# Kernel tuning notes

Measured on AMD Instinct MI355X. Metric: run time of the kernel, lower is better.

The kernel has to match this reference:

```python
import jax, jax.numpy as jnp
import numpy as np

NEG_SLOPE = 0.2
NUM_GRAPHS = 1000


def gatv2_layer(x, src, dst, Wl, bl, Wr, br, att, bias, heads, outc, concat):
    # PyG GATv2Conv (eval mode, dropout inactive, self-loops already appended)
    N = x.shape[0]
    xl = (x @ Wl + bl).reshape(N, heads, outc)   # source transform
    xr = (x @ Wr + br).reshape(N, heads, outc)   # target transform
    e = jax.nn.leaky_relu(xl[src] + xr[dst], NEG_SLOPE)      # [E,H,C]
    logit = jnp.einsum('ehc,hc->eh', e, att)                  # [E,H]
    m = jax.ops.segment_max(logit, dst, num_segments=N)      # segment softmax over dst
    ex = jnp.exp(logit - m[dst])
    denom = jax.ops.segment_sum(ex, dst, num_segments=N)
    alpha = ex / denom[dst]                                   # [E,H]
    out = jax.ops.segment_sum(xl[src] * alpha[:, :, None], dst, num_segments=N)  # [N,H,C]
    out = out.reshape(N, heads * outc) if concat else out.mean(axis=1)
    return out + bias


def _glorot(key, shape, scale=0.05):
    return jax.random.normal(key, shape, dtype=jnp.float32) * scale


def setup_inputs() -> dict:
    key = jax.random.key(0)
    ks = jax.random.split(key, 24)
    N, E = 50000, 800000
    Din, Hc, H, Dout = 64, 64, 4, 128
    inp = {
        'x': jax.random.normal(ks[0], (N, Din), dtype=jnp.float32),
        'edge_index': jax.random.randint(ks[1], (2, E), 0, N, dtype=jnp.int32),
        'batch': jnp.sort(jax.random.randint(ks[2], (N,), 0, NUM_GRAPHS, dtype=jnp.int32)),
        # layer 1: Din -> H*Hc (concat)
        'Wl1': _glorot(ks[3], (Din, H * Hc)), 'bl1': jnp.zeros((H * Hc,), jnp.float32),
        'Wr1': _glorot(ks[4], (Din, H * Hc)), 'br1': jnp.zeros((H * Hc,), jnp.float32),
        'att1': _glorot(ks[5], (H, Hc)), 'b1': jnp.zeros((H * Hc,), jnp.float32),
        # layer 2: H*Hc -> H*Hc (concat)
        'Wl2': _glorot(ks[6], (H * Hc, H * Hc)), 'bl2': jnp.zeros((H * Hc,), jnp.float32),
        'Wr2': _glorot(ks[7], (H * Hc, H * Hc)), 'br2': jnp.zeros((H * Hc,), jnp.float32),
        'att2': _glorot(ks[8], (H, Hc)), 'b2': jnp.zeros((H * Hc,), jnp.float32),
        # layer 3: H*Hc -> Dout, 1 head, concat=False
        'Wl3': _glorot(ks[9], (H * Hc, Dout)), 'bl3': jnp.zeros((Dout,), jnp.float32),
        'Wr3': _glorot(ks[10], (H * Hc, Dout)), 'br3': jnp.zeros((Dout,), jnp.float32),
        'att3': _glorot(ks[11], (1, Dout)), 'b3': jnp.zeros((Dout,), jnp.float32),
    }
    return inp


def reference(x, edge_index, batch, Wl1, bl1, Wr1, br1, att1, b1,
              Wl2, bl2, Wr2, br2, att2, b2, Wl3, bl3, Wr3, br3, att3, b3):
    N = x.shape[0]
    loops = jnp.arange(N, dtype=edge_index.dtype)
    src = jnp.concatenate([edge_index[0], loops])  # add_self_loops=True
    dst = jnp.concatenate([edge_index[1], loops])
    h = gatv2_layer(x, src, dst, Wl1, bl1, Wr1, br1, att1, b1, 4, 64, True)
    h = jax.nn.elu(h)
    h = gatv2_layer(h, src, dst, Wl2, bl2, Wr2, br2, att2, b2, 4, 64, True)
    h = jax.nn.elu(h)
    h = gatv2_layer(h, src, dst, Wl3, bl3, Wr3, br3, att3, b3, 1, 128, False)
    # global mean pool over graphs
    sums = jax.ops.segment_sum(h, batch, num_segments=NUM_GRAPHS)
    cnt = jax.ops.segment_sum(jnp.ones((N,), h.dtype), batch, num_segments=NUM_GRAPHS)
    return sums / jnp.clip(cnt, 1.0)[:, None]
```

## Files before the change

kernel.cpp:

```cpp
#include <hip/hip_runtime.h>
#include <math.h>

#define NEG_SLOPE 0.2f

typedef _Float16 half8 __attribute__((ext_vector_type(8)));
typedef _Float16 half4 __attribute__((ext_vector_type(4)));
typedef _Float16 half2v __attribute__((ext_vector_type(2)));
typedef float    f32x4 __attribute__((ext_vector_type(4)));
typedef float    fvec4 __attribute__((ext_vector_type(4)));
typedef float    fvec2 __attribute__((ext_vector_type(2)));

__global__ void k_count(const int* __restrict__ dst, int E, int N, int* __restrict__ cnt){
  int i = blockIdx.x*blockDim.x + threadIdx.x;
  if (i < E) atomicAdd(&cnt[dst[i]], 1);
  else if (i < E + N) atomicAdd(&cnt[i - E], 1);
}

__global__ void k_scan_block(const int* __restrict__ cnt, int* __restrict__ ex,
                             int* __restrict__ bsum, int N){
  __shared__ int tmp[256];
  int t = threadIdx.x;
  int i = blockIdx.x*256 + t;
  int v = (i < N) ? cnt[i] : 0;
  tmp[t] = v; __syncthreads();
  for (int off = 1; off < 256; off <<= 1){
    int u = (t >= off) ? tmp[t-off] : 0;
    __syncthreads();
    tmp[t] += u;
    __syncthreads();
  }
  if (i < N) ex[i] = tmp[t] - v;
  if (t == 255) bsum[blockIdx.x] = tmp[255];
}

__global__ void k_scan_tops(int* __restrict__ bsum, int nb){
  __shared__ int tmp[256];
  int t = threadIdx.x;
  int v = (t < nb) ? bsum[t] : 0;
  tmp[t] = v; __syncthreads();
  for (int off = 1; off < 256; off <<= 1){
    int u = (t >= off) ? tmp[t-off] : 0;
    __syncthreads();
    tmp[t] += u;
    __syncthreads();
  }
  if (t < nb) bsum[t] = tmp[t] - v;
}

__global__ void k_scan_add(int* __restrict__ row_start, const int* __restrict__ bsum,
                           int N, int total){
  int i = blockIdx.x*256 + threadIdx.x;
  if (i < N) row_start[i] += bsum[blockIdx.x];
  if (i == 0) row_start[N] = total;
}

__global__ void k_scatter(const int* __restrict__ src, const int* __restrict__ dst,
                          int E, int N, const int* __restrict__ row_start,
                          int* __restrict__ cursor, int* __restrict__ edge_src){
  int i = blockIdx.x*blockDim.x + threadIdx.x;
  if (i < E){
    int d = dst[i];
    int p = atomicAdd(&cursor[d], 1);
    edge_src[row_start[d] + p] = src[i];
  } else if (i < E + N){
    int n = i - E;
    int p = atomicAdd(&cursor[n], 1);
    edge_src[row_start[n] + p] = n;
  }
}

__global__ void k_splitW(const float* __restrict__ W, _Float16* __restrict__ WT,
                         int K, int Nw){
  int id = blockIdx.x*blockDim.x + threadIdx.x;
  if (id >= K*Nw) return;
  int n = id / K, k = id % K;
  float w = W[(size_t)k*Nw + n];
  _Float16 h = (_Float16)w;
  _Float16 l = (_Float16)(w - (float)h);
  size_t base = (size_t)n*2*K;
  WT[base + k]     = h;
  WT[base + K + k] = l;
}

__global__ void k_split_x(const float* __restrict__ x, _Float16* __restrict__ X16,
                          int N, int K){
  int id = blockIdx.x*blockDim.x + threadIdx.x;
  int per = K/8;
  if (id >= N*per) return;
  int rr = id / per, c = (id % per)*8;
  fvec4 f0 = *(const fvec4*)&x[(size_t)rr*K + c];
  fvec4 f1 = *(const fvec4*)&x[(size_t)rr*K + c + 4];
  half8 hh, hl;
  #pragma unroll
  for (int q = 0; q < 4; ++q){
    _Float16 h0 = (_Float16)f0[q];
    hh[q] = h0; hl[q] = (_Float16)(f0[q] - (float)h0);
    _Float16 h1 = (_Float16)f1[q];
    hh[4+q] = h1; hl[4+q] = (_Float16)(f1[q] - (float)h1);
  }
  *(half8*)&X16[(size_t)rr*2*K + c]     = hh;
  *(half8*)&X16[(size_t)rr*2*K + K + c] = hl;
}

__global__ __launch_bounds__(256, 2)
void k_gemm_split(const _Float16* __restrict__ A16, const _Float16* __restrict__ WT,
                  const float* __restrict__ biasL, const float* __restrict__ biasR,
                  _Float16* __restrict__ XL, _Float16* __restrict__ XR,
                  int M, int K, int NwHalf, int gy, int qq, int rr){
  __shared__ _Float16 sAh[128*72];
  __shared__ _Float16 sAl[128*72];
  __shared__ _Float16 sWh[128*72];
  __shared__ _Float16 sWl[128*72];
  const int tid  = threadIdx.x;
  const int lane = tid & 63;
  const int wid  = tid >> 6;
  const int wm   = wid >> 1, wn = wid & 1;

  const int h   = blockIdx.x;
  const int xcd = h & 7, idx = h >> 3;
  const int l   = xcd*qq + (xcd < rr ? xcd : rr) + idx;
  const int bx  = l / gy, by = l - bx*gy;
  const int m0  = bx * 128;
  const int n0  = by * 128;
  const int lda = 2*K;

  f32x4 acc[4][4];
  #pragma unroll
  for (int i = 0; i < 4; ++i)
    #pragma unroll
    for (int j = 0; j < 4; ++j)
      acc[i][j] = (f32x4){0.f,0.f,0.f,0.f};

  const int l15 = lane & 15;
  const int lhi = lane >> 4;

  const int nc = K/64;
  for (int c = 0; c < nc; ++c){
    const int kA = c*64;
    #pragma unroll
    for (int it = 0; it < 4; ++it){
      int idx2 = it*256 + tid;
      int r = idx2 >> 3, c8 = idx2 & 7;
      int gr = m0 + r;
      half8 vh = (half8)(_Float16)0.f, vl = (half8)(_Float16)0.f;
      if (gr < M){
        vh = *(const half8*)&A16[(size_t)gr*lda + kA + c8*8];
        vl = *(const half8*)&A16[(size_t)gr*lda + K + kA + c8*8];
      }
      *(half8*)&sAh[r*72 + c8*8] = vh;
      *(half8*)&sAl[r*72 + c8*8] = vl;
      int wr = n0 + r;
      *(half8*)&sWh[r*72 + c8*8] = *(const half8*)&WT[(size_t)wr*lda + kA + c8*8];
      *(half8*)&sWl[r*72 + c8*8] = *(const half8*)&WT[(size_t)wr*lda + K + kA + c8*8];
    }
    __syncthreads();
    #pragma unroll
    for (int ks = 0; ks < 64; ks += 32){
      half8 ah[4], al[4], bh[4], bl[4];
      #pragma unroll
      for (int fm = 0; fm < 4; ++fm){
        ah[fm] = *(const half8*)&sAh[(wm*64 + fm*16 + l15)*72 + ks + 8*lhi];
        al[fm] = *(const half8*)&sAl[(wm*64 + fm*16 + l15)*72 + ks + 8*lhi];
      }
      #pragma unroll
      for (int fn = 0; fn < 4; ++fn){
        bh[fn] = *(const half8*)&sWh[(wn*64 + fn*16 + l15)*72 + ks + 8*lhi];
        bl[fn] = *(const half8*)&sWl[(wn*64 + fn*16 + l15)*72 + ks + 8*lhi];
      }
      #pragma unroll
      for (int fm = 0; fm < 4; ++fm)
        #pragma unroll
        for (int fn = 0; fn < 4; ++fn)
          acc[fm][fn] = __builtin_amdgcn_mfma_f32_16x16x32_f16(ah[fm], bh[fn], acc[fm][fn], 0, 0, 0);
      #pragma unroll
      for (int fm = 0; fm < 4; ++fm)
        #pragma unroll
        for (int fn = 0; fn < 4; ++fn)
          acc[fm][fn] = __builtin_amdgcn_mfma_f32_16x16x32_f16(al[fm], bh[fn], acc[fm][fn], 0, 0, 0);
      #pragma unroll
      for (int fm = 0; fm < 4; ++fm)
        #pragma unroll
        for (int fn = 0; fn < 4; ++fn)
          acc[fm][fn] = __builtin_amdgcn_mfma_f32_16x16x32_f16(ah[fm], bl[fn], acc[fm][fn], 0, 0, 0);
    }
    __syncthreads();
  }
  const bool isR = (n0 >= NwHalf);
  const float* bias = isR ? biasR : biasL;
  _Float16* Xo = isR ? XR : XL;
  const int nbase = isR ? (n0 - NwHalf) : n0;
  #pragma unroll
  for (int fm = 0; fm < 4; ++fm){
    #pragma unroll
    for (int fn = 0; fn < 4; ++fn){
      int cc = nbase + wn*64 + fn*16 + l15;
      float bv = bias[cc];
      #pragma unroll
      for (int q = 0; q < 4; ++q){
        int row = m0 + wm*64 + fm*16 + lhi*4 + q;
        if (row < M) Xo[(size_t)row*NwHalf + cc] = (_Float16)(acc[fm][fn][q] + bv);
      }
    }
  }
}

template<int HC, int C, int SPLIT>
__global__ __launch_bounds__(256) void k_gat_agg(const _Float16* __restrict__ xl,
                                                 const _Float16* __restrict__ xr,
                                                 const float* __restrict__ att,
                                                 const float* __restrict__ bias,
                                                 const int* __restrict__ row_start,
                                                 const int* __restrict__ edge_src,
                                                 void* __restrict__ outp,
                                                 int N, int apply_elu){
  constexpr int VEC   = 8;
  constexpr int LPE   = HC/VEC;
  constexpr int EPW   = 64/LPE;
  constexpr int GROUP = C/VEC;
  const float M_INIT = -1.0e30f, T_INACT = -2.0e30f, THR = 11.54f;

  int wid = (int)(((size_t)blockIdx.x * blockDim.x + threadIdx.x) >> 6);
  int lane = threadIdx.x & 63;
  if (wid >= N) return;
  const int h  = lane / LPE;
  const int li = lane % LPE;
  const int ch = (li/GROUP)*C + (li%GROUP)*VEC;

  const _Float16 s16 = (_Float16)NEG_SLOPE;
  const half2v slope2 = {s16, s16};

  half2v attv2[4], xrr2[4];
  {
    fvec4 a0 = *(const fvec4*)&att[ch];
    fvec4 a1 = *(const fvec4*)&att[ch+4];
    const float L2E = 1.4426950408889634f;
    attv2[0][0]=(_Float16)(a0[0]*L2E); attv2[0][1]=(_Float16)(a0[1]*L2E);
    attv2[1][0]=(_Float16)(a0[2]*L2E); attv2[1][1]=(_Float16)(a0[3]*L2E);
    attv2[2][0]=(_Float16)(a1[0]*L2E); attv2[2][1]=(_Float16)(a1[1]*L2E);
    attv2[3][0]=(_Float16)(a1[2]*L2E); attv2[3][1]=(_Float16)(a1[3]*L2E);
    half8 hv = *(const half8*)&xr[(unsigned)(wid*HC) + ch];
    #pragma unroll
    for (int p = 0; p < 4; ++p){ xrr2[p][0] = hv[2*p]; xrr2[p][1] = hv[2*p+1]; }
  }

  float acc[VEC];
  #pragma unroll
  for (int q = 0; q < VEC; ++q) acc[q] = 0.f;
  float m = M_INIT, s = 0.f;

  const int e0   = row_start[wid];
  const int ecnt = row_start[wid+1] - e0;
  const _Float16* xlb = xl + ch;

  auto rowload = [&](int sn)->half8 {
    return *(const half8*)(xlb + (unsigned)(sn*HC));
  };
  auto logit1 = [&](half8 x8)->float{
    float t = 0.f;
    #pragma unroll
    for (int p = 0; p < 4; ++p){
      half2v xp; xp[0] = x8[2*p]; xp[1] = x8[2*p+1];
      half2v v  = xp + xrr2[p];
      half2v lv = __builtin_elementwise_max(v, v*slope2);
      t = __builtin_amdgcn_fdot2(lv, attv2[p], t, false);
    }
    #pragma unroll
    for (int off = GROUP/2; off > 0; off >>= 1)
      t += __shfl_xor(t, off, 64);
    return t;
  };
  auto update2 = [&](float ta, float tb, half8 xa, half8 xb){
    float pm = fmaxf(ta, tb);
    if (__all(pm <= m + THR)){
      float pa = __builtin_amdgcn_exp2f(ta - m);
      float pb = __builtin_amdgcn_exp2f(tb - m);
      s += pa + pb;
      #pragma unroll
      for (int q = 0; q < VEC; ++q)
        acc[q] = fmaf(pa, (float)xa[q], fmaf(pb, (float)xb[q], acc[q]));
    } else {
      float nm = fmaxf(pm, m);
      float wo = __builtin_amdgcn_exp2f(m - nm);
      float pa = __builtin_amdgcn_exp2f(ta - nm);
      float pb = __builtin_amdgcn_exp2f(tb - nm);
      s = fmaf(s, wo, pa + pb);
      m = nm;
      #pragma unroll
      for (int q = 0; q < VEC; ++q)
        acc[q] = fmaf(pa, (float)xa[q], fmaf(pb, (float)xb[q], acc[q]*wo));
    }
  };

  int base = e0 + h;
  const int R = ecnt / (2*EPW);
  for (int r = 0; r < R; ++r, base += 2*EPW){
    int sa = edge_src[base];
    int sb = edge_src[base + EPW];
    half8 xa = rowload(sa);
    half8 xb = rowload(sb);
    float ta = logit1(xa);
    float tb = logit1(xb);
    update2(ta, tb, xa, xb);
  }
  if (2*EPW*R < ecnt){
    const int last = e0 + ecnt;
    bool a1 = base < last, a2 = base + EPW < last;
    int sa = a1 ? edge_src[base] : 0;
    int sb = a2 ? edge_src[base + EPW] : 0;
    half8 xa = rowload(sa);
    half8 xb = rowload(sb);
    float ta = logit1(xa); ta = a1 ? ta : T_INACT;
    float tb = logit1(xb); tb = a2 ? tb : T_INACT;
    update2(ta, tb, xa, xb);
  }

  #pragma unroll
  for (int off = LPE; off < 64; off <<= 1){
    float mo = __shfl_xor(m, off, 64);
    float so = __shfl_xor(s, off, 64);
    float M  = fmaxf(m, mo);
    float w  = __builtin_amdgcn_exp2f(m  - M);
    float wo = __builtin_amdgcn_exp2f(mo - M);
    s = s*w + so*wo;
    #pragma unroll
    for (int q = 0; q < VEC; ++q)
      acc[q] = acc[q]*w + __shfl_xor(acc[q], off, 64)*wo;
    m = M;
  }

  if (h == 0){
    float inv = 1.f / s;
    fvec4 b0 = *(const fvec4*)&bias[ch];
    fvec4 b1 = *(const fvec4*)&bias[ch+4];
    float ov[VEC];
    #pragma unroll
    for (int q = 0; q < VEC; ++q){
      float o = acc[q]*inv + (q < 4 ? b0[q] : b1[q-4]);
      if (apply_elu) o = (o > 0.f) ? o : (__expf(o) - 1.f);
      ov[q] = o;
    }
    if constexpr (SPLIT){
      _Float16* o16 = (_Float16*)outp;
      half8 hh, hl;
      #pragma unroll
      for (int q = 0; q < VEC; ++q){
        _Float16 hv = (_Float16)ov[q];
        hh[q] = hv; hl[q] = (_Float16)(ov[q] - (float)hv);
      }
      *(half8*)&o16[(unsigned)(wid*2*HC) + ch]      = hh;
      *(half8*)&o16[(unsigned)(wid*2*HC) + HC + ch] = hl;
    } else {
      float* o32 = (float*)outp;
      *(fvec4*)&o32[(unsigned)(wid*HC) + ch]     = (fvec4){ov[0],ov[1],ov[2],ov[3]};
      *(fvec4*)&o32[(unsigned)(wid*HC) + ch + 4] = (fvec4){ov[4],ov[5],ov[6],ov[7]};
    }
  }
}

__global__ void k_pool(const float* __restrict__ h, const int* __restrict__ batch,
                       float* __restrict__ pool, int* __restrict__ gcnt, int N){
  int wid = (int)(((size_t)blockIdx.x * blockDim.x + threadIdx.x) >> 6);
  int lane = threadIdx.x & 63;
  if (wid >= N) return;
  int g = batch[wid];
  #pragma unroll
  for (int j = 0; j < 2; ++j)
    atomicAdd(&pool[(size_t)g*128 + j*64 + lane], h[(size_t)wid*128 + j*64 + lane]);
  if (lane == 0) atomicAdd(&gcnt[g], 1);
}

__global__ void k_pool_div(const float* __restrict__ pool, const int* __restrict__ gcnt,
                           float* __restrict__ out, int total){
  int i = blockIdx.x*blockDim.x + threadIdx.x;
  if (i < total) out[i] = pool[i] / fmaxf((float)gcnt[i >> 7], 1.f);
}

extern "C" void kernel_launch(void* const* d_in, const int* in_sizes, int n_in,
                              void* d_out, int out_size, void* d_ws, size_t ws_size,
                              hipStream_t stream){
  const float* x    = (const float*)d_in[0];
  const int*   ei   = (const int*)  d_in[1];
  const int*   batch= (const int*)  d_in[2];
  const float* Wl1  = (const float*)d_in[3];
  const float* bl1  = (const float*)d_in[4];
  const float* Wr1  = (const float*)d_in[5];
  const float* br1  = (const float*)d_in[6];
  const float* att1 = (const float*)d_in[7];
  const float* b1   = (const float*)d_in[8];
  const float* Wl2  = (const float*)d_in[9];
  const float* bl2  = (const float*)d_in[10];
  const float* Wr2  = (const float*)d_in[11];
  const float* br2  = (const float*)d_in[12];
  const float* att2 = (const float*)d_in[13];
  const float* b2   = (const float*)d_in[14];
  const float* Wl3  = (const float*)d_in[15];
  const float* bl3  = (const float*)d_in[16];
  const float* Wr3  = (const float*)d_in[17];
  const float* br3  = (const float*)d_in[18];
  const float* att3 = (const float*)d_in[19];
  const float* b3   = (const float*)d_in[20];

  int N  = in_sizes[2];
  int E  = in_sizes[1] / 2;
  int NG = out_size / 128;
  const int* esrc = ei;
  const int* edst = ei + E;
  int Mpad = ((N + 127)/128)*128;

  size_t off = 0;
  char* base = (char*)d_ws;
  auto alloc = [&](size_t bytes)->void*{
    void* p = base + off;
    off += (bytes + 255) & ~(size_t)255;
    return p;
  };
  _Float16* XL  = (_Float16*)alloc((size_t)Mpad*256*sizeof(_Float16));
  _Float16* XR  = (_Float16*)alloc((size_t)Mpad*256*sizeof(_Float16));
  _Float16* Hsp = (_Float16*)alloc((size_t)Mpad*512*sizeof(_Float16));
  _Float16* X16 = (_Float16*)alloc((size_t)Mpad*128*sizeof(_Float16));
  float*    Hb32= (float*)   alloc((size_t)Mpad*128*sizeof(float));
  _Float16* WT  = (_Float16*)alloc((size_t)512*512*sizeof(_Float16));
  int* row_start = (int*)alloc(((size_t)N+1)*sizeof(int));
  int* edge_src  = (int*)alloc((size_t)(E+N)*sizeof(int));
  int* cnt       = (int*)alloc((size_t)N*sizeof(int));
  int* bsum      = (int*)alloc(256*sizeof(int));
  float* pool    = (float*)alloc((size_t)NG*128*sizeof(float));
  int* gcnt      = (int*)alloc((size_t)NG*sizeof(int));
  (void)ws_size; (void)n_in;

  int EN = E + N;
  int nb = (N + 255) / 256;

  hipMemsetAsync(cnt, 0, (size_t)N*sizeof(int), stream);
  k_count<<<(EN+255)/256, 256, 0, stream>>>(edst, E, N, cnt);
  k_scan_block<<<nb, 256, 0, stream>>>(cnt, row_start, bsum, N);
  k_scan_tops<<<1, 256, 0, stream>>>(bsum, nb);
  k_scan_add<<<nb, 256, 0, stream>>>(row_start, bsum, N, EN);
  hipMemsetAsync(cnt, 0, (size_t)N*sizeof(int), stream);
  k_scatter<<<(EN+255)/256, 256, 0, stream>>>(esrc, edst, E, N, row_start, cnt, edge_src);

  dim3 blk(256);
  int agg_blocks = (N + 3) / 4;
  int gx = Mpad/128;
  int G1 = gx*4;
  int G3 = gx*2;

  k_splitW<<<(64*256+255)/256, blk, 0, stream>>>(Wl1, WT,           64, 256);
  k_splitW<<<(64*256+255)/256, blk, 0, stream>>>(Wr1, WT + 256*128, 64, 256);
  k_split_x<<<((N*8)+255)/256, blk, 0, stream>>>(x, X16, N, 64);
  k_gemm_split<<<G1, blk, 0, stream>>>(X16, WT, bl1, br1, XL, XR, N, 64, 256, 4, G1/8, G1%8);
  k_gat_agg<256,64,1><<<agg_blocks, blk, 0, stream>>>(XL, XR, att1, b1, row_start, edge_src, Hsp, N, 1);

  k_splitW<<<(256*256+255)/256, blk, 0, stream>>>(Wl2, WT,           256, 256);
  k_splitW<<<(256*256+255)/256, blk, 0, stream>>>(Wr2, WT + 256*512, 256, 256);
  k_gemm_split<<<G1, blk, 0, stream>>>(Hsp, WT, bl2, br2, XL, XR, N, 256, 256, 4, G1/8, G1%8);
  k_gat_agg<256,64,1><<<agg_blocks, blk, 0, stream>>>(XL, XR, att2, b2, row_start, edge_src, Hsp, N, 1);

  k_splitW<<<(256*128+255)/256, blk, 0, stream>>>(Wl3, WT,           256, 128);
  k_splitW<<<(256*128+255)/256, blk, 0, stream>>>(Wr3, WT + 128*512, 256, 128);
  k_gemm_split<<<G3, blk, 0, stream>>>(Hsp, WT, bl3, br3, XL, XR, N, 256, 128, 2, G3/8, G3%8);
  k_gat_agg<128,128,0><<<agg_blocks, blk, 0, stream>>>(XL, XR, att3, b3, row_start, edge_src, Hb32, N, 0);

  hipMemsetAsync(pool, 0, (size_t)NG*128*sizeof(float), stream);
  hipMemsetAsync(gcnt, 0, (size_t)NG*sizeof(int), stream);
  k_pool<<<agg_blocks, blk, 0, stream>>>(Hb32, batch, pool, gcnt, N);
  k_pool_div<<<(NG*128+255)/256, 256, 0, stream>>>(pool, gcnt, (float*)d_out, NG*128);
}
```

Baseline: 500.9 us.

## Drop activation split-precision, fuse pooling into last aggregation, merge weight-split launches

Activations are now stored as a single fp16 copy instead of an fp16 hi/lo pair, so the GEMM runs two MFMA passes instead of three and reads half the A data. Weights keep their hi/lo split. The final GAT aggregation atomically accumulates straight into the pooled buffer, with the bias added in the divide step, which removes the fp32 intermediate and the separate pool kernel. The two weight-split launches per layer are merged into one. The cost is lower accuracy on activations and more atomic contention on the pool buffer.

```diff
diff --git a/kernel.cpp b/kernel.cpp
--- a/kernel.cpp
+++ b/kernel.cpp
@@ -69,37 +69,37 @@
   }
 }
 
-__global__ void k_splitW(const float* __restrict__ W, _Float16* __restrict__ WT,
-                         int K, int Nw){
+__global__ void k_splitW2(const float* __restrict__ WL, const float* __restrict__ WR,
+                          _Float16* __restrict__ WT, int K, int Nw){
   int id = blockIdx.x*blockDim.x + threadIdx.x;
-  if (id >= K*Nw) return;
-  int n = id / K, k = id % K;
+  if (id >= 2*K*Nw) return;
+  int half = id / (K*Nw);
+  int rem  = id - half*K*Nw;
+  int n = rem / K, k = rem % K;
+  const float* W = half ? WR : WL;
   float w = W[(size_t)k*Nw + n];
   _Float16 h = (_Float16)w;
   _Float16 l = (_Float16)(w - (float)h);
-  size_t base = (size_t)n*2*K;
+  size_t base = (size_t)(half*Nw + n)*2*K;
   WT[base + k]     = h;
   WT[base + K + k] = l;
 }
 
-__global__ void k_split_x(const float* __restrict__ x, _Float16* __restrict__ X16,
-                          int N, int K){
+__global__ void k_cvt_x(const float* __restrict__ x, _Float16* __restrict__ X16,
+                        int N, int K){
   int id = blockIdx.x*blockDim.x + threadIdx.x;
   int per = K/8;
   if (id >= N*per) return;
   int rr = id / per, c = (id % per)*8;
   fvec4 f0 = *(const fvec4*)&x[(size_t)rr*K + c];
   fvec4 f1 = *(const fvec4*)&x[(size_t)rr*K + c + 4];
-  half8 hh, hl;
+  half8 hh;
   #pragma unroll
   for (int q = 0; q < 4; ++q){
-    _Float16 h0 = (_Float16)f0[q];
-    hh[q] = h0; hl[q] = (_Float16)(f0[q] - (float)h0);
-    _Float16 h1 = (_Float16)f1[q];
-    hh[4+q] = h1; hl[4+q] = (_Float16)(f1[q] - (float)h1);
-  }
-  *(half8*)&X16[(size_t)rr*2*K + c]     = hh;
-  *(half8*)&X16[(size_t)rr*2*K + K + c] = hl;
+    hh[q]   = (_Float16)f0[q];
+    hh[4+q] = (_Float16)f1[q];
+  }
+  *(half8*)&X16[(size_t)rr*K + c] = hh;
 }
 
 __global__ __launch_bounds__(256, 2)
@@ -107,8 +107,7 @@
                   const float* __restrict__ biasL, const float* __restrict__ biasR,
                   _Float16* __restrict__ XL, _Float16* __restrict__ XR,
                   int M, int K, int NwHalf, int gy, int qq, int rr){
-  __shared__ _Float16 sAh[128*72];
-  __shared__ _Float16 sAl[128*72];
+  __shared__ _Float16 sA [128*72];
   __shared__ _Float16 sWh[128*72];
   __shared__ _Float16 sWl[128*72];
   const int tid  = threadIdx.x;
@@ -122,7 +121,7 @@
   const int bx  = l / gy, by = l - bx*gy;
   const int m0  = bx * 128;
   const int n0  = by * 128;
-  const int lda = 2*K;
+  const int ldw = 2*K;
 
   f32x4 acc[4][4];
   #pragma unroll
@@ -142,26 +141,20 @@
       int idx2 = it*256 + tid;
       int r = idx2 >> 3, c8 = idx2 & 7;
       int gr = m0 + r;
-      half8 vh = (half8)(_Float16)0.f, vl = (half8)(_Float16)0.f;
-      if (gr < M){
-        vh = *(const half8*)&A16[(size_t)gr*lda + kA + c8*8];
-        vl = *(const half8*)&A16[(size_t)gr*lda + K + kA + c8*8];
-      }
-      *(half8*)&sAh[r*72 + c8*8] = vh;
-      *(half8*)&sAl[r*72 + c8*8] = vl;
+      half8 va = (half8)(_Float16)0.f;
+      if (gr < M) va = *(const half8*)&A16[(size_t)gr*K + kA + c8*8];
+      *(half8*)&sA[r*72 + c8*8] = va;
       int wr = n0 + r;
-      *(half8*)&sWh[r*72 + c8*8] = *(const half8*)&WT[(size_t)wr*lda + kA + c8*8];
-      *(half8*)&sWl[r*72 + c8*8] = *(const half8*)&WT[(size_t)wr*lda + K + kA + c8*8];
+      *(half8*)&sWh[r*72 + c8*8] = *(const half8*)&WT[(size_t)wr*ldw + kA + c8*8];
+      *(half8*)&sWl[r*72 + c8*8] = *(const half8*)&WT[(size_t)wr*ldw + K + kA + c8*8];
     }
     __syncthreads();
     #pragma unroll
     for (int ks = 0; ks < 64; ks += 32){
-      half8 ah[4], al[4], bh[4], bl[4];
-      #pragma unroll
-      for (int fm = 0; fm < 4; ++fm){
-        ah[fm] = *(const half8*)&sAh[(wm*64 + fm*16 + l15)*72 + ks + 8*lhi];
-        al[fm] = *(const half8*)&sAl[(wm*64 + fm*16 + l15)*72 + ks + 8*lhi];
-      }
+      half8 a[4], bh[4], bl[4];
+      #pragma unroll
+      for (int fm = 0; fm < 4; ++fm)
+        a[fm] = *(const half8*)&sA[(wm*64 + fm*16 + l15)*72 + ks + 8*lhi];
       #pragma unroll
       for (int fn = 0; fn < 4; ++fn){
         bh[fn] = *(const half8*)&sWh[(wn*64 + fn*16 + l15)*72 + ks + 8*lhi];
@@ -171,17 +164,12 @@
       for (int fm = 0; fm < 4; ++fm)
         #pragma unroll
         for (int fn = 0; fn < 4; ++fn)
-          acc[fm][fn] = __builtin_amdgcn_mfma_f32_16x16x32_f16(ah[fm], bh[fn], acc[fm][fn], 0, 0, 0);
+          acc[fm][fn] = __builtin_amdgcn_mfma_f32_16x16x32_f16(a[fm], bh[fn], acc[fm][fn], 0, 0, 0);
       #pragma unroll
       for (int fm = 0; fm < 4; ++fm)
         #pragma unroll
         for (int fn = 0; fn < 4; ++fn)
-          acc[fm][fn] = __builtin_amdgcn_mfma_f32_16x16x32_f16(al[fm], bh[fn], acc[fm][fn], 0, 0, 0);
-      #pragma unroll
-      for (int fm = 0; fm < 4; ++fm)
-        #pragma unroll
-        for (int fn = 0; fn < 4; ++fn)
-          acc[fm][fn] = __builtin_amdgcn_mfma_f32_16x16x32_f16(ah[fm], bl[fn], acc[fm][fn], 0, 0, 0);
+          acc[fm][fn] = __builtin_amdgcn_mfma_f32_16x16x32_f16(a[fm], bl[fn], acc[fm][fn], 0, 0, 0);
     }
     __syncthreads();
   }
@@ -204,14 +192,16 @@
   }
 }
 
-template<int HC, int C, int SPLIT>
+template<int HC, int C, int POOL>
 __global__ __launch_bounds__(256) void k_gat_agg(const _Float16* __restrict__ xl,
                                                  const _Float16* __restrict__ xr,
                                                  const float* __restrict__ att,
                                                  const float* __restrict__ bias,
                                                  const int* __restrict__ row_start,
                                                  const int* __restrict__ edge_src,
+                                                 const int* __restrict__ batch,
                                                  void* __restrict__ outp,
+                                                 int* __restrict__ gcnt,
                                                  int N, int apply_elu){
   constexpr int VEC   = 8;
   constexpr int LPE   = HC/VEC;
@@ -330,49 +320,33 @@
 
   if (h == 0){
     float inv = 1.f / s;
-    fvec4 b0 = *(const fvec4*)&bias[ch];
-    fvec4 b1 = *(const fvec4*)&bias[ch+4];
-    float ov[VEC];
-    #pragma unroll
-    for (int q = 0; q < VEC; ++q){
-      float o = acc[q]*inv + (q < 4 ? b0[q] : b1[q-4]);
-      if (apply_elu) o = (o > 0.f) ? o : (__expf(o) - 1.f);
-      ov[q] = o;
-    }
-    if constexpr (SPLIT){
-      _Float16* o16 = (_Float16*)outp;
-      half8 hh, hl;
+    if constexpr (!POOL){
+      fvec4 b0 = *(const fvec4*)&bias[ch];
+      fvec4 b1 = *(const fvec4*)&bias[ch+4];
+      half8 hh;
       #pragma unroll
       for (int q = 0; q < VEC; ++q){
-        _Float16 hv = (_Float16)ov[q];
-        hh[q] = hv; hl[q] = (_Float16)(ov[q] - (float)hv);
+        float o = acc[q]*inv + (q < 4 ? b0[q] : b1[q-4]);
+        if (apply_elu) o = (o > 0.f) ? o : (__expf(o) - 1.f);
+        hh[q] = (_Float16)o;
       }
-      *(half8*)&o16[(unsigned)(wid*2*HC) + ch]      = hh;
-      *(half8*)&o16[(unsigned)(wid*2*HC) + HC + ch] = hl;
+      *(half8*)&((_Float16*)outp)[(unsigned)(wid*HC) + ch] = hh;
     } else {
-      float* o32 = (float*)outp;
-      *(fvec4*)&o32[(unsigned)(wid*HC) + ch]     = (fvec4){ov[0],ov[1],ov[2],ov[3]};
-      *(fvec4*)&o32[(unsigned)(wid*HC) + ch + 4] = (fvec4){ov[4],ov[5],ov[6],ov[7]};
-    }
-  }
-}
-
-__global__ void k_pool(const float* __restrict__ h, const int* __restrict__ batch,
-                       float* __restrict__ pool, int* __restrict__ gcnt, int N){
-  int wid = (int)(((size_t)blockIdx.x * blockDim.x + threadIdx.x) >> 6);
-  int lane = threadIdx.x & 63;
-  if (wid >= N) return;
-  int g = batch[wid];
-  #pragma unroll
-  for (int j = 0; j < 2; ++j)
-    atomicAdd(&pool[(size_t)g*128 + j*64 + lane], h[(size_t)wid*128 + j*64 + lane]);
-  if (lane == 0) atomicAdd(&gcnt[g], 1);
+      int g = batch[wid];
+      float* pool = (float*)outp;
+      #pragma unroll
+      for (int q = 0; q < VEC; ++q)
+        atomicAdd(&pool[(unsigned)(g*HC) + ch + q], acc[q]*inv);
+      if (li == 0) atomicAdd(&gcnt[g], 1);
+    }
+  }
 }
 
 __global__ void k_pool_div(const float* __restrict__ pool, const int* __restrict__ gcnt,
-                           float* __restrict__ out, int total){
+                           const float* __restrict__ bias, float* __restrict__ out,
+                           int total){
   int i = blockIdx.x*blockDim.x + threadIdx.x;
-  if (i < total) out[i] = pool[i] / fmaxf((float)gcnt[i >> 7], 1.f);
+  if (i < total) out[i] = pool[i] / fmaxf((float)gcnt[i >> 7], 1.f) + bias[i & 127];
 }
 
 extern "C" void kernel_launch(void* const* d_in, const int* in_sizes, int n_in,
@@ -416,9 +390,8 @@
   };
   _Float16* XL  = (_Float16*)alloc((size_t)Mpad*256*sizeof(_Float16));
   _Float16* XR  = (_Float16*)alloc((size_t)Mpad*256*sizeof(_Float16));
-  _Float16* Hsp = (_Float16*)alloc((size_t)Mpad*512*sizeof(_Float16));
-  _Float16* X16 = (_Float16*)alloc((size_t)Mpad*128*sizeof(_Float16));
-  float*    Hb32= (float*)   alloc((size_t)Mpad*128*sizeof(float));
+  _Float16* H16 = (_Float16*)alloc((size_t)Mpad*256*sizeof(_Float16));
+  _Float16* X16 = (_Float16*)alloc((size_t)Mpad*64*sizeof(_Float16));
   _Float16* WT  = (_Float16*)alloc((size_t)512*512*sizeof(_Float16));
   int* row_start = (int*)alloc(((size_t)N+1)*sizeof(int));
   int* edge_src  = (int*)alloc((size_t)(E+N)*sizeof(int));
@@ -438,6 +411,8 @@
   k_scan_add<<<nb, 256, 0, stream>>>(row_start, bsum, N, EN);
   hipMemsetAsync(cnt, 0, (size_t)N*sizeof(int), stream);
   k_scatter<<<(EN+255)/256, 256, 0, stream>>>(esrc, edst, E, N, row_start, cnt, edge_src);
+  hipMemsetAsync(pool, 0, (size_t)NG*128*sizeof(float), stream);
+  hipMemsetAsync(gcnt, 0, (size_t)NG*sizeof(int), stream);
 
   dim3 blk(256);
   int agg_blocks = (N + 3) / 4;
@@ -445,24 +420,18 @@
   int G1 = gx*4;
   int G3 = gx*2;
 
-  k_splitW<<<(64*256+255)/256, blk, 0, stream>>>(Wl1, WT,           64, 256);
-  k_splitW<<<(64*256+255)/256, blk, 0, stream>>>(Wr1, WT + 256*128, 64, 256);
-  k_split_x<<<((N*8)+255)/256, blk, 0, stream>>>(x, X16, N, 64);
+  k_splitW2<<<(2*64*256+255)/256, blk, 0, stream>>>(Wl1, Wr1, WT, 64, 256);
+  k_cvt_x<<<((N*8)+255)/256, blk, 0, stream>>>(x, X16, N, 64);
   k_gemm_split<<<G1, blk, 0, stream>>>(X16, WT, bl1, br1, XL, XR, N, 64, 256, 4, G1/8, G1%8);
-  k_gat_agg<256,64,1><<<agg_blocks, blk, 0, stream>>>(XL, XR, att1, b1, row_start, edge_src, Hsp, N, 1);
-
-  k_splitW<<<(256*256+255)/256, blk, 0, stream>>>(Wl2, WT,           256, 256);
-  k_splitW<<<(256*256+255)/256, blk, 0, stream>>>(Wr2, WT + 256*512, 256, 256);
-  k_gemm_split<<<G1, blk, 0, stream>>>(Hsp, WT, bl2, br2, XL, XR, N, 256, 256, 4, G1/8, G1%8);
-  k_gat_agg<256,64,1><<<agg_blocks, blk, 0, stream>>>(XL, XR, att2, b2, row_start, edge_src, Hsp, N, 1);
-
-  k_splitW<<<(256*128+255)/256, blk, 0, stream>>>(Wl3, WT,           256, 128);
-  k_splitW<<<(256*128+255)/256, blk, 0, stream>>>(Wr3, WT + 128*512, 256, 128);
-  k_gemm_split<<<G3, blk, 0, stream>>>(Hsp, WT, bl3, br3, XL, XR, N, 256, 128, 2, G3/8, G3%8);
-  k_gat_agg<128,128,0><<<agg_blocks, blk, 0, stream>>>(XL, XR, att3, b3, row_start, edge_src, Hb32, N, 0);
-
-  hipMemsetAsync(pool, 0, (size_t)NG*128*sizeof(float), stream);
-  hipMemsetAsync(gcnt, 0, (size_t)NG*sizeof(int), stream);
-  k_pool<<<agg_blocks, blk, 0, stream>>>(Hb32, batch, pool, gcnt, N);
-  k_pool_div<<<(NG*128+255)/256, 256, 0, stream>>>(pool, gcnt, (float*)d_out, NG*128);
-}
+  k_gat_agg<256,64,0><<<agg_blocks, blk, 0, stream>>>(XL, XR, att1, b1, row_start, edge_src, batch, H16, gcnt, N, 1);
+
+  k_splitW2<<<(2*256*256+255)/256, blk, 0, stream>>>(Wl2, Wr2, WT, 256, 256);
+  k_gemm_split<<<G1, blk, 0, stream>>>(H16, WT, bl2, br2, XL, XR, N, 256, 256, 4, G1/8, G1%8);
+  k_gat_agg<256,64,0><<<agg_blocks, blk, 0, stream>>>(XL, XR, att2, b2, row_start, edge_src, batch, H16, gcnt, N, 1);
+
+  k_splitW2<<<(2*256*128+255)/256, blk, 0, stream>>>(Wl3, Wr3, WT, 256, 128);
+  k_gemm_split<<<G3, blk, 0, stream>>>(H16, WT, bl3, br3, XL, XR, N, 256, 128, 2, G3/8, G3%8);
+  k_gat_agg<128,128,1><<<agg_blocks, blk, 0, stream>>>(XL, XR, att3, b3, row_start, edge_src, batch, pool, gcnt, N, 0);
+
+  k_pool_div<<<(NG*128+255)/256, 256, 0, stream>>>(pool, gcnt, b3, (float*)d_out, NG*128);
+}
```

After: 615.9 us. 23.0% more time.
